# Kernel optimization log

Hardware: AMD Instinct MI355X
Metric: run time of the kernel (lower is better)

## Reference

```python
import jax, jax.numpy as jnp
import numpy as np

N_NODES = 100000
N_EDGES = 1000000
N_LABEL = 200000
D_IN = 128
D_HID = 128


def setup_inputs() -> dict:
    key = jax.random.key(0)
    k1, k2, k3, k4, k5 = jax.random.split(key, 5)
    node_feature = jax.random.normal(k1, (N_NODES, D_IN), dtype=jnp.float32)
    edge_index = jax.random.randint(k2, (2, N_EDGES), 0, N_NODES, dtype=jnp.int64)
    edge_label_index = jax.random.randint(k3, (2, N_LABEL), 0, N_NODES, dtype=jnp.int64)
    W1 = jax.random.normal(k4, (D_IN, D_HID), dtype=jnp.float32) * (1.0 / np.sqrt(D_IN))
    b1 = jnp.zeros((D_HID,), dtype=jnp.float32)
    W2 = jax.random.normal(k5, (D_HID, D_HID), dtype=jnp.float32) * (1.0 / np.sqrt(D_HID))
    b2 = jnp.zeros((D_HID,), dtype=jnp.float32)
    return {"node_feature": node_feature, "edge_index": edge_index,
            "edge_label_index": edge_label_index,
            "W1": W1, "b1": b1, "W2": W2, "b2": b2}


def reference(node_feature, edge_index, edge_label_index, W1, b1, W2, b2):
    N = node_feature.shape[0]
    # GCN normalization with added self-loops (PyG GCNConv default)
    loop = jnp.arange(N, dtype=edge_index.dtype)
    src = jnp.concatenate([edge_index[0], loop])  # [E+N]
    dst = jnp.concatenate([edge_index[1], loop])  # [E+N]
    deg = jax.ops.segment_sum(jnp.ones_like(dst, dtype=node_feature.dtype), dst, N)
    dinv = jnp.where(deg > 0, jax.lax.rsqrt(deg), 0.0)
    norm = dinv[src] * dinv[dst]  # [E+N]

    def gcn_conv(x, W, b):
        h = x @ W                              # [N, d] transform first (d small)
        msg = h[src] * norm[:, None]           # gather + scale over edges
        return jax.ops.segment_sum(msg, dst, N) + b  # scatter-add to targets

    # eval mode: dropout(p=0.2) is identity
    x = jax.nn.relu(gcn_conv(node_feature, W1, b1))
    x = gcn_conv(x, W2, b2)

    # edge scoring: gather both endpoints, elementwise mul, sum over features
    nodes_first = x[edge_label_index[0]]
    nodes_second = x[edge_label_index[1]]
    pred = jnp.sum(nodes_first * nodes_second, axis=-1)  # [N_LABEL]
    return pred
```

## Files before the change

### kernel.cpp

```cpp
#include <hip/hip_runtime.h>
#include <hip/hip_bf16.h>


#define N_NODES 100000
#define N_EDGES 1000000
#define N_LABEL 200000
#define D_FEAT 128
#define BM 128

#define NB 782
#define BCAP 2048
#define P1_EPT 16
#define P1_BLOCKS 245

typedef short bf16x8 __attribute__((ext_vector_type(8)));
typedef float f32x4 __attribute__((ext_vector_type(4)));

__device__ inline unsigned int f2bf(float x) {
    unsigned int u = __float_as_uint(x);
    return (u + 0x7FFFu + ((u >> 16) & 1u)) >> 16;
}
__device__ inline unsigned int bf16pack(float a, float b) {
    return f2bf(a) | (f2bf(b) << 16);
}
__device__ inline float bflo(unsigned int u) { return __uint_as_float(u << 16); }
__device__ inline float bfhi(unsigned int u) { return __uint_as_float(u & 0xFFFF0000u); }

__global__ __launch_bounds__(256) void pass1_bucket_w2bf(
    const int* __restrict__ src, const int* __restrict__ dst,
    int* __restrict__ gcur, unsigned int* __restrict__ temp,
    const float* __restrict__ W1, const float* __restrict__ W2,
    unsigned short* __restrict__ Wt1, unsigned short* __restrict__ Wt2) {
    int b = blockIdx.x, t = threadIdx.x;
    if (b >= P1_BLOCKS) {
        int i = (b - P1_BLOCKS) * 256 + t;
        const float* W = (i < 16384) ? W1 : W2;
        unsigned short* Wt = (i < 16384) ? Wt1 : Wt2;
        int j = i & 16383;
        int n = j >> 7, k = j & 127;
        Wt[j] = (unsigned short)f2bf(W[(size_t)k * 128 + n]);
        return;
    }
    __shared__ int hist[NB], base[NB];
    for (int i = t; i < NB; i += 256) hist[i] = 0;
    __syncthreads();

    int se[P1_EPT], de[P1_EPT], rk[P1_EPT];
    int e0 = b * (P1_EPT * 256) + t;
#pragma unroll
    for (int j = 0; j < P1_EPT; ++j) {
        int e = e0 + j * 256;
        if (e < N_EDGES) {
            se[j] = src[e];
            de[j] = dst[e];
            rk[j] = atomicAdd(&hist[de[j] >> 7], 1);
        }
    }
    __syncthreads();
    for (int i = t; i < NB; i += 256) {
        int h = hist[i];
        base[i] = h ? atomicAdd(&gcur[i], h) : 0;
    }
    __syncthreads();
#pragma unroll
    for (int j = 0; j < P1_EPT; ++j) {
        int e = e0 + j * 256;
        if (e < N_EDGES) {
            int k = de[j] >> 7;
            int pos = base[k] + rk[j];
            if (pos < BCAP)
                temp[(size_t)k * BCAP + pos] =
                    (unsigned int)(((de[j] & 127) << 17) | se[j]);
        }
    }
}

template <bool BF16_IN>
__device__ __forceinline__ void gemm_body(const void* __restrict__ Xv,
                                          const unsigned short* __restrict__ Wt,
                                          unsigned int* __restrict__ Y,
                                          int nrows, int bid, short* Ws) {
    int t = threadIdx.x;
#pragma unroll
    for (int i = 0; i < 8; ++i) {
        int c = i * 256 + t;
        int n = c >> 4, q = c & 15;
        uint4 v = *(const uint4*)&Wt[(size_t)n * 128 + q * 8];
        *(uint4*)&Ws[n * 128 + ((q ^ (n & 15)) << 3)] = v;
    }
    __syncthreads();

    int wv = t >> 6;
    int lane = t & 63, l16 = lane & 15, quad = lane >> 4;
    int rbase = bid * BM + wv * 32;

    f32x4 acc[2][8];
#pragma unroll
    for (int rt = 0; rt < 2; ++rt)
#pragma unroll
        for (int nt = 0; nt < 8; ++nt) acc[rt][nt] = (f32x4){0.f, 0.f, 0.f, 0.f};

#pragma unroll
    for (int kb = 0; kb < 4; ++kb) {
        bf16x8 af[2];
#pragma unroll
        for (int rt = 0; rt < 2; ++rt) {
            int row = rbase + rt * 16 + l16;
            if (row > nrows - 1) row = nrows - 1;
            if constexpr (BF16_IN) {
                const unsigned int* Xb = (const unsigned int*)Xv;
                af[rt] = *(const bf16x8*)&Xb[(size_t)row * 64 + kb * 16 + quad * 4];
            } else {
                const float* X = (const float*)Xv;
                float4 fa = ((const float4*)X)[(size_t)row * 32 + kb * 8 + quad * 2];
                float4 fb = ((const float4*)X)[(size_t)row * 32 + kb * 8 + quad * 2 + 1];
                union { uint4 u; bf16x8 v; } cv;
                cv.u.x = bf16pack(fa.x, fa.y);
                cv.u.y = bf16pack(fa.z, fa.w);
                cv.u.z = bf16pack(fb.x, fb.y);
                cv.u.w = bf16pack(fb.z, fb.w);
                af[rt] = cv.v;
            }
        }
        bf16x8 bfr[8];
#pragma unroll
        for (int nt = 0; nt < 8; ++nt) {
            int n = nt * 16 + l16;
            bfr[nt] = *(const bf16x8*)&Ws[n * 128 + (((kb * 4 + quad) ^ l16) << 3)];
        }
#pragma unroll
        for (int rt = 0; rt < 2; ++rt)
#pragma unroll
            for (int nt = 0; nt < 8; ++nt)
                acc[rt][nt] = __builtin_amdgcn_mfma_f32_16x16x32_bf16(
                    af[rt], bfr[nt], acc[rt][nt], 0, 0, 0);
    }

    short* Ys = (short*)Y;
#pragma unroll
    for (int rt = 0; rt < 2; ++rt)
#pragma unroll
        for (int reg = 0; reg < 4; ++reg) {
            int row = rbase + rt * 16 + quad * 4 + reg;
            if (row < nrows) {
#pragma unroll
                for (int nt = 0; nt < 8; ++nt)
                    Ys[(size_t)row * 128 + nt * 16 + l16] = (short)f2bf(acc[rt][nt][reg]);
            }
        }
}

__global__ __launch_bounds__(256) void gemm128_mfma_bf16(const unsigned int* __restrict__ Xb,
                                                         const unsigned short* __restrict__ Wt,
                                                         unsigned int* __restrict__ Y,
                                                         int nrows) {
    __shared__ __align__(16) short Ws[128 * 128];
    gemm_body<true>(Xb, Wt, Y, nrows, blockIdx.x, Ws);
}

#define G_GEMM 782
__global__ __launch_bounds__(256) void fused_gemm1_pass2(
    const float* __restrict__ feat, const unsigned short* __restrict__ wt1,
    unsigned int* __restrict__ Hb, const int* __restrict__ gcur,
    const unsigned int* __restrict__ temp, int* __restrict__ row_ptr,
    float* __restrict__ dinv, int* __restrict__ packed) {
    __shared__ __align__(16) short Ws[128 * 128];
    int b = blockIdx.x, t = threadIdx.x;
    if (b < G_GEMM) {
        gemm_body<false>(feat, wt1, Hb, N_NODES, b, Ws);
        return;
    }
    int k = b - G_GEMM;
    unsigned int* ed = (unsigned int*)Ws;
    int* hist = (int*)(ed + BCAP);
    int* rp = hist + 128;
    int* cur = rp + 128;
    int* sc = cur + 128;
    int* red = sc + 128;

    int part = 0;
    for (int j = t; j < NB; j += 256)
        if (j < k) part += gcur[j];
    red[t] = part;
    __syncthreads();
    for (int off = 128; off > 0; off >>= 1) {
        if (t < off) red[t] += red[t + off];
        __syncthreads();
    }
    int gbase = red[0];
    int nk = gcur[k];
    if (nk > BCAP) nk = BCAP;

    if (t < 128) { hist[t] = 0; cur[t] = 0; }
    __syncthreads();
    for (int i = t; i < nk; i += 256) {
        unsigned int v = temp[(size_t)k * BCAP + i];
        ed[i] = v;
        atomicAdd(&hist[v >> 17], 1);
    }
    __syncthreads();

    if (t < 128) sc[t] = hist[t];
    __syncthreads();
    for (int off = 1; off < 128; off <<= 1) {
        int a = (t < 128 && t >= off) ? sc[t - off] : 0;
        __syncthreads();
        if (t < 128) sc[t] += a;
        __syncthreads();
    }
    if (t < 128) {
        rp[t] = sc[t] - hist[t];
        int n = k * 128 + t;
        if (n < N_NODES) {
            row_ptr[n] = gbase + rp[t];
            dinv[n] = rsqrtf((float)(hist[t] + 1));
        }
    }
    if (k == NB - 1 && t == 0) row_ptr[N_NODES] = N_EDGES;
    __syncthreads();

    for (int i = t; i < nk; i += 256) {
        unsigned int v = ed[i];
        int dl = v >> 17;
        int r = atomicAdd(&cur[dl], 1);
        packed[gbase + rp[dl] + r] = (int)(v & 0x1FFFF);
    }
}

template <bool RELU>
__global__ __launch_bounds__(256) void aggregate(const unsigned int* __restrict__ Hb,
                                                 const int* __restrict__ packed,
                                                 const int* __restrict__ row_ptr,
                                                 const float* __restrict__ dinv,
                                                 const float* __restrict__ bias,
                                                 unsigned int* __restrict__ Xb) {
    int v0 = blockIdx.x * 8 + (threadIdx.x >> 6) * 2;
    int v1 = v0 + 1;
    int lane = threadIdx.x & 63;
    if (v0 >= N_NODES) return;
    bool h1 = (v1 < N_NODES);

    int st0 = row_ptr[v0], en0 = row_ptr[v0 + 1];
    int st1 = h1 ? row_ptr[v1] : 0, en1 = h1 ? row_ptr[v1 + 1] : 0;
    float dv0 = dinv[v0];
    float dv1 = h1 ? dinv[v1] : 0.f;

    unsigned int su0 = Hb[(size_t)v0 * 64 + lane];
    float a0 = dv0 * bflo(su0), a1 = dv0 * bfhi(su0);
    unsigned int su1 = h1 ? Hb[(size_t)v1 * 64 + lane] : 0u;
    float b0 = dv1 * bflo(su1), b1 = dv1 * bfhi(su1);

    for (int c0 = st0, c1 = st1; c0 < en0 || c1 < en1; c0 += 32, c1 += 32) {
        int n0 = en0 - c0; n0 = n0 < 0 ? 0 : (n0 > 32 ? 32 : n0);
        int n1 = en1 - c1; n1 = n1 < 0 ? 0 : (n1 > 32 ? 32 : n1);
        int p = 0;
        float d = 0.f;
        if (lane < 32) {
            if (lane < n0) { p = packed[c0 + lane]; d = dinv[p]; }
        } else {
            if (lane - 32 < n1) { p = packed[c1 + lane - 32]; d = dinv[p]; }
        }
        int nmax = n0 > n1 ? n0 : n1;
        for (int j = 0; j < nmax; j += 8) {
            int sA[8], sB[8];
            float dA[8], dB[8];
#pragma unroll
            for (int q = 0; q < 8; ++q) {
                sA[q] = __shfl(p, j + q);
                dA[q] = __shfl(d, j + q);
                sB[q] = __shfl(p, 32 + j + q);
                dB[q] = __shfl(d, 32 + j + q);
            }
            unsigned int uA[8], uB[8];
#pragma unroll
            for (int q = 0; q < 8; ++q) {
                uA[q] = Hb[(size_t)sA[q] * 64 + lane];
                uB[q] = Hb[(size_t)sB[q] * 64 + lane];
            }
#pragma unroll
            for (int q = 0; q < 8; ++q) {
                a0 = fmaf(dA[q], bflo(uA[q]), a0);
                a1 = fmaf(dA[q], bfhi(uA[q]), a1);
                b0 = fmaf(dB[q], bflo(uB[q]), b0);
                b1 = fmaf(dB[q], bfhi(uB[q]), b1);
            }
        }
    }

    float2 bb = ((const float2*)bias)[lane];
    a0 = fmaf(a0, dv0, bb.x);
    a1 = fmaf(a1, dv0, bb.y);
    b0 = fmaf(b0, dv1, bb.x);
    b1 = fmaf(b1, dv1, bb.y);
    if (RELU) {
        a0 = fmaxf(a0, 0.f);
        a1 = fmaxf(a1, 0.f);
        b0 = fmaxf(b0, 0.f);
        b1 = fmaxf(b1, 0.f);
    }
    Xb[(size_t)v0 * 64 + lane] = bf16pack(a0, a1);
    if (h1) Xb[(size_t)v1 * 64 + lane] = bf16pack(b0, b1);
}

__global__ __launch_bounds__(256) void score_kernel(const int* __restrict__ ea,
                                                    const int* __restrict__ eb,
                                                    const unsigned int* __restrict__ Xb,
                                                    float* __restrict__ out) {
    int wbase = (blockIdx.x * 4 + (threadIdx.x >> 6)) * 4;
    int lane = threadIdx.x & 63;
    if (wbase >= N_LABEL) return;
    int ne = N_LABEL - wbase;
    if (ne > 4) ne = 4;

    unsigned int ua[4], ub[4];
#pragma unroll
    for (int e = 0; e < 4; ++e)
        if (e < ne) {
            int ia = ea[wbase + e], ib = eb[wbase + e];
            ua[e] = Xb[(size_t)ia * 64 + lane];
            ub[e] = Xb[(size_t)ib * 64 + lane];
        }
#pragma unroll
    for (int e = 0; e < 4; ++e)
        if (e < ne) {
            float p = bflo(ua[e]) * bflo(ub[e]) + bfhi(ua[e]) * bfhi(ub[e]);
#pragma unroll
            for (int off = 32; off > 0; off >>= 1) p += __shfl_down(p, off);
            if (lane == 0) out[wbase + e] = p;
        }
}

extern "C" void kernel_launch(void* const* d_in, const int* in_sizes, int n_in,
                              void* d_out, int out_size, void* d_ws, size_t ws_size,
                              hipStream_t stream) {
    const float* feat = (const float*)d_in[0];
    const int* ei = (const int*)d_in[1];
    const int* eli = (const int*)d_in[2];
    const float* W1 = (const float*)d_in[3];
    const float* b1 = (const float*)d_in[4];
    const float* W2 = (const float*)d_in[5];
    const float* b2 = (const float*)d_in[6];
    float* out = (float*)d_out;

    const int* src = ei;
    const int* dst = ei + N_EDGES;
    const int* la = eli;
    const int* lb = eli + N_LABEL;

    int* gcur = (int*)d_ws;
    int* row_ptr = gcur + 1024;
    float* dinv = (float*)(row_ptr + N_NODES + 4);
    unsigned short* wt1 = (unsigned short*)(dinv + N_NODES);
    unsigned short* wt2 = wt1 + 16384;
    int* packed = (int*)(wt2 + 16384);
    unsigned int* Hb = (unsigned int*)(packed + N_EDGES);
    unsigned int* Xb = Hb + (size_t)N_NODES * 64;
    unsigned int* temp = Xb;

    const int TB = 256;
    int gGemm = (N_NODES + BM - 1) / BM;
    int gAgg = (N_NODES + 7) / 8;
    int gScore = (N_LABEL + 15) / 16;

    hipMemsetAsync(gcur, 0, NB * sizeof(int), stream);

    pass1_bucket_w2bf<<<P1_BLOCKS + 128, TB, 0, stream>>>(src, dst, gcur, temp,
                                                          W1, W2, wt1, wt2);

    fused_gemm1_pass2<<<G_GEMM + NB, TB, 0, stream>>>(feat, wt1, Hb, gcur, temp,
                                                      row_ptr, dinv, packed);

    aggregate<true><<<gAgg, TB, 0, stream>>>(Hb, packed, row_ptr, dinv, b1, Xb);

    gemm128_mfma_bf16<<<gGemm, TB, 0, stream>>>(Xb, wt2, Hb, N_NODES);
    aggregate<false><<<gAgg, TB, 0, stream>>>(Hb, packed, row_ptr, dinv, b2, Xb);

    score_kernel<<<gScore, TB, 0, stream>>>(la, lb, Xb, out);
}
```

Baseline: 282.4 us.

## Fuse GEMM1 with edge bucketing and convert W1 inline, split sort pass

GEMM1 now reads W1 as fp32 and converts it to bf16 while staging it into shared memory, so the separate W1 transpose/convert step is gone. Edge bucketing (pass1) and the W2 conversion now run in the same launch as GEMM1, and the per-bucket sort becomes its own kernel. The aim is to overlap the bandwidth-bound bucketing with the GEMM and keep the launch count the same. The cost is that every GEMM block does strided fp32 reads of W1, and the shared-memory allocation is sized for the GEMM, which may lower occupancy for the bucketing blocks. A minor reorder in aggregate issues the degree shuffles after the gathers.

Result: slower. 303.0 us (+7.3%).

```diff
diff --git a/kernel.cpp b/kernel.cpp
--- a/kernel.cpp
+++ b/kernel.cpp
@@ -12,6 +12,8 @@
 #define BCAP 2048
 #define P1_EPT 16
 #define P1_BLOCKS 245
+#define G_GEMM 782
+#define G_W2BF 64
 
 typedef short bf16x8 __attribute__((ext_vector_type(8)));
 typedef float f32x4 __attribute__((ext_vector_type(4)));
@@ -26,58 +28,9 @@
 __device__ inline float bflo(unsigned int u) { return __uint_as_float(u << 16); }
 __device__ inline float bfhi(unsigned int u) { return __uint_as_float(u & 0xFFFF0000u); }
 
-__global__ __launch_bounds__(256) void pass1_bucket_w2bf(
-    const int* __restrict__ src, const int* __restrict__ dst,
-    int* __restrict__ gcur, unsigned int* __restrict__ temp,
-    const float* __restrict__ W1, const float* __restrict__ W2,
-    unsigned short* __restrict__ Wt1, unsigned short* __restrict__ Wt2) {
-    int b = blockIdx.x, t = threadIdx.x;
-    if (b >= P1_BLOCKS) {
-        int i = (b - P1_BLOCKS) * 256 + t;
-        const float* W = (i < 16384) ? W1 : W2;
-        unsigned short* Wt = (i < 16384) ? Wt1 : Wt2;
-        int j = i & 16383;
-        int n = j >> 7, k = j & 127;
-        Wt[j] = (unsigned short)f2bf(W[(size_t)k * 128 + n]);
-        return;
-    }
-    __shared__ int hist[NB], base[NB];
-    for (int i = t; i < NB; i += 256) hist[i] = 0;
-    __syncthreads();
-
-    int se[P1_EPT], de[P1_EPT], rk[P1_EPT];
-    int e0 = b * (P1_EPT * 256) + t;
-#pragma unroll
-    for (int j = 0; j < P1_EPT; ++j) {
-        int e = e0 + j * 256;
-        if (e < N_EDGES) {
-            se[j] = src[e];
-            de[j] = dst[e];
-            rk[j] = atomicAdd(&hist[de[j] >> 7], 1);
-        }
-    }
-    __syncthreads();
-    for (int i = t; i < NB; i += 256) {
-        int h = hist[i];
-        base[i] = h ? atomicAdd(&gcur[i], h) : 0;
-    }
-    __syncthreads();
-#pragma unroll
-    for (int j = 0; j < P1_EPT; ++j) {
-        int e = e0 + j * 256;
-        if (e < N_EDGES) {
-            int k = de[j] >> 7;
-            int pos = base[k] + rk[j];
-            if (pos < BCAP)
-                temp[(size_t)k * BCAP + pos] =
-                    (unsigned int)(((de[j] & 127) << 17) | se[j]);
-        }
-    }
-}
-
-template <bool BF16_IN>
+template <bool BF16_IN, bool F32W>
 __device__ __forceinline__ void gemm_body(const void* __restrict__ Xv,
-                                          const unsigned short* __restrict__ Wt,
+                                          const void* __restrict__ Wsrc,
                                           unsigned int* __restrict__ Y,
                                           int nrows, int bid, short* Ws) {
     int t = threadIdx.x;
@@ -85,8 +38,27 @@
     for (int i = 0; i < 8; ++i) {
         int c = i * 256 + t;
         int n = c >> 4, q = c & 15;
-        uint4 v = *(const uint4*)&Wt[(size_t)n * 128 + q * 8];
-        *(uint4*)&Ws[n * 128 + ((q ^ (n & 15)) << 3)] = v;
+        if constexpr (F32W) {
+            const float* Wf = (const float*)Wsrc;
+            union { uint4 u; bf16x8 v; } cv;
+            float f0 = Wf[(q * 8 + 0) * 128 + n];
+            float f1 = Wf[(q * 8 + 1) * 128 + n];
+            float f2 = Wf[(q * 8 + 2) * 128 + n];
+            float f3 = Wf[(q * 8 + 3) * 128 + n];
+            float f4 = Wf[(q * 8 + 4) * 128 + n];
+            float f5 = Wf[(q * 8 + 5) * 128 + n];
+            float f6 = Wf[(q * 8 + 6) * 128 + n];
+            float f7 = Wf[(q * 8 + 7) * 128 + n];
+            cv.u.x = bf16pack(f0, f1);
+            cv.u.y = bf16pack(f2, f3);
+            cv.u.z = bf16pack(f4, f5);
+            cv.u.w = bf16pack(f6, f7);
+            *(uint4*)&Ws[n * 128 + ((q ^ (n & 15)) << 3)] = cv.u;
+        } else {
+            const unsigned short* Wt = (const unsigned short*)Wsrc;
+            uint4 v = *(const uint4*)&Wt[(size_t)n * 128 + q * 8];
+            *(uint4*)&Ws[n * 128 + ((q ^ (n & 15)) << 3)] = v;
+        }
     }
     __syncthreads();
 
@@ -150,33 +122,68 @@
         }
 }
 
-__global__ __launch_bounds__(256) void gemm128_mfma_bf16(const unsigned int* __restrict__ Xb,
-                                                         const unsigned short* __restrict__ Wt,
-                                                         unsigned int* __restrict__ Y,
-                                                         int nrows) {
-    __shared__ __align__(16) short Ws[128 * 128];
-    gemm_body<true>(Xb, Wt, Y, nrows, blockIdx.x, Ws);
-}
-
-#define G_GEMM 782
-__global__ __launch_bounds__(256) void fused_gemm1_pass2(
-    const float* __restrict__ feat, const unsigned short* __restrict__ wt1,
-    unsigned int* __restrict__ Hb, const int* __restrict__ gcur,
-    const unsigned int* __restrict__ temp, int* __restrict__ row_ptr,
-    float* __restrict__ dinv, int* __restrict__ packed) {
+__global__ __launch_bounds__(256) void fused_front(
+    const float* __restrict__ feat, const float* __restrict__ W1,
+    unsigned int* __restrict__ Hb,
+    const int* __restrict__ src, const int* __restrict__ dst,
+    int* __restrict__ gcur, unsigned int* __restrict__ temp,
+    const float* __restrict__ W2, unsigned short* __restrict__ wt2) {
     __shared__ __align__(16) short Ws[128 * 128];
     int b = blockIdx.x, t = threadIdx.x;
     if (b < G_GEMM) {
-        gemm_body<false>(feat, wt1, Hb, N_NODES, b, Ws);
+        gemm_body<false, true>(feat, W1, Hb, N_NODES, b, Ws);
         return;
     }
-    int k = b - G_GEMM;
-    unsigned int* ed = (unsigned int*)Ws;
-    int* hist = (int*)(ed + BCAP);
-    int* rp = hist + 128;
-    int* cur = rp + 128;
-    int* sc = cur + 128;
-    int* red = sc + 128;
+    b -= G_GEMM;
+    if (b >= P1_BLOCKS) {
+        int i = (b - P1_BLOCKS) * 256 + t;
+        int n = i >> 7, k = i & 127;
+        wt2[i] = (unsigned short)f2bf(W2[(size_t)k * 128 + n]);
+        return;
+    }
+    int* hist = (int*)Ws;
+    int* base = hist + NB;
+    for (int i = t; i < NB; i += 256) hist[i] = 0;
+    __syncthreads();
+
+    int se[P1_EPT], de[P1_EPT], rk[P1_EPT];
+    int e0 = b * (P1_EPT * 256) + t;
+#pragma unroll
+    for (int j = 0; j < P1_EPT; ++j) {
+        int e = e0 + j * 256;
+        if (e < N_EDGES) {
+            se[j] = src[e];
+            de[j] = dst[e];
+            rk[j] = atomicAdd(&hist[de[j] >> 7], 1);
+        }
+    }
+    __syncthreads();
+    for (int i = t; i < NB; i += 256) {
+        int h = hist[i];
+        base[i] = h ? atomicAdd(&gcur[i], h) : 0;
+    }
+    __syncthreads();
+#pragma unroll
+    for (int j = 0; j < P1_EPT; ++j) {
+        int e = e0 + j * 256;
+        if (e < N_EDGES) {
+            int k = de[j] >> 7;
+            int pos = base[k] + rk[j];
+            if (pos < BCAP)
+                temp[(size_t)k * BCAP + pos] =
+                    (unsigned int)(((de[j] & 127) << 17) | se[j]);
+        }
+    }
+}
+
+__global__ __launch_bounds__(256) void pass2_sort(
+    const int* __restrict__ gcur, const unsigned int* __restrict__ temp,
+    int* __restrict__ row_ptr, float* __restrict__ dinv,
+    int* __restrict__ packed) {
+    int k = blockIdx.x, t = threadIdx.x;
+    __shared__ unsigned int ed[BCAP];
+    __shared__ int hist[128], rp[128], cur[128], sc[128];
+    __shared__ int red[256];
 
     int part = 0;
     for (int j = t; j < NB; j += 256)
@@ -225,6 +232,14 @@
         int r = atomicAdd(&cur[dl], 1);
         packed[gbase + rp[dl] + r] = (int)(v & 0x1FFFF);
     }
+}
+
+__global__ __launch_bounds__(256) void gemm128_mfma_bf16(const unsigned int* __restrict__ Xb,
+                                                         const unsigned short* __restrict__ Wt,
+                                                         unsigned int* __restrict__ Y,
+                                                         int nrows) {
+    __shared__ __align__(16) short Ws[128 * 128];
+    gemm_body<true, false>(Xb, Wt, Y, nrows, blockIdx.x, Ws);
 }
 
 template <bool RELU>
@@ -263,19 +278,22 @@
         int nmax = n0 > n1 ? n0 : n1;
         for (int j = 0; j < nmax; j += 8) {
             int sA[8], sB[8];
-            float dA[8], dB[8];
 #pragma unroll
             for (int q = 0; q < 8; ++q) {
                 sA[q] = __shfl(p, j + q);
-                dA[q] = __shfl(d, j + q);
                 sB[q] = __shfl(p, 32 + j + q);
-                dB[q] = __shfl(d, 32 + j + q);
             }
             unsigned int uA[8], uB[8];
 #pragma unroll
             for (int q = 0; q < 8; ++q) {
                 uA[q] = Hb[(size_t)sA[q] * 64 + lane];
                 uB[q] = Hb[(size_t)sB[q] * 64 + lane];
+            }
+            float dA[8], dB[8];
+#pragma unroll
+            for (int q = 0; q < 8; ++q) {
+                dA[q] = __shfl(d, j + q);
+                dB[q] = __shfl(d, 32 + j + q);
             }
 #pragma unroll
             for (int q = 0; q < 8; ++q) {
@@ -350,8 +368,7 @@
     int* gcur = (int*)d_ws;
     int* row_ptr = gcur + 1024;
     float* dinv = (float*)(row_ptr + N_NODES + 4);
-    unsigned short* wt1 = (unsigned short*)(dinv + N_NODES);
-    unsigned short* wt2 = wt1 + 16384;
+    unsigned short* wt2 = (unsigned short*)(dinv + N_NODES);
     int* packed = (int*)(wt2 + 16384);
     unsigned int* Hb = (unsigned int*)(packed + N_EDGES);
     unsigned int* Xb = Hb + (size_t)N_NODES * 64;
@@ -364,11 +381,10 @@
 
     hipMemsetAsync(gcur, 0, NB * sizeof(int), stream);
 
-    pass1_bucket_w2bf<<<P1_BLOCKS + 128, TB, 0, stream>>>(src, dst, gcur, temp,
-                                                          W1, W2, wt1, wt2);
-
-    fused_gemm1_pass2<<<G_GEMM + NB, TB, 0, stream>>>(feat, wt1, Hb, gcur, temp,
-                                                      row_ptr, dinv, packed);
+    fused_front<<<G_GEMM + P1_BLOCKS + G_W2BF, TB, 0, stream>>>(
+        feat, W1, Hb, src, dst, gcur, temp, W2, wt2);
+
+    pass2_sort<<<NB, TB, 0, stream>>>(gcur, temp, row_ptr, dinv, packed);
 
     aggregate<true><<<gAgg, TB, 0, stream>>>(Hb, packed, row_ptr, dinv, b1, Xb);
 
```
